# Kernel optimization log

Measured on AMD Instinct MI355X. Metric: run time of the kernel, lower is better.

Reference implementation:

```python
import jax, jax.numpy as jnp
import numpy as np

TEMPERATURE = 0.07
ALPHA = 1.0
SIGMOID_SCALE = 1.0
EPS = 1e-8

BSZ, N_VIEWS, D = 256, 2, 128


def setup_inputs() -> dict:
    key = jax.random.key(0)
    k1, k2, k3 = jax.random.split(key, 3)
    features = jax.random.normal(k1, (BSZ, N_VIEWS, D), dtype=jnp.float32)
    labels = jax.random.uniform(k2, (BSZ,), dtype=jnp.float32)  # continuous positions
    v_prog = jax.random.normal(k3, (D,), dtype=jnp.float32)     # learned direction param
    return {"features": features, "labels": labels, "v_prog": v_prog}


def _l2_normalize(x, axis, eps=1e-12):
    # matches F.normalize: x / clamp_min(||x||, eps)
    n = jnp.linalg.norm(x, axis=axis, keepdims=True)
    return x / jnp.maximum(n, eps)


def reference(features, labels, v_prog):
    bsz, n_views, d = features.shape
    # contrast_mode='all': torch.cat(torch.unbind(features, dim=1), dim=0)
    cf = jnp.concatenate([features[:, v] for v in range(n_views)], axis=0)  # (n, d)
    pos = jnp.tile(labels.reshape(-1, 1), (n_views, 1))                      # (n, 1)
    n = cf.shape[0]

    # ---------------- RAL loss ----------------
    f = _l2_normalize(cf, axis=1)
    sim = (f @ f.T) / TEMPERATURE                 # (n, n)
    pd = jnp.abs(pos - pos.T)                     # (n, n) |p_i - p_j|
    exp_sim = jnp.exp(sim)
    not_i = ~jnp.eye(n, dtype=bool)               # exclude k == i
    # mask3[i, j, k] = (pd[i,k] >= pd[i,j]) & (k != i)
    mask3 = (pd[:, None, :] >= pd[:, :, None]) & not_i[:, None, :]
    # denominator[i, j] = sum_k exp_sim[i, k] * mask3[i, j, k]  (fused masked reduction)
    denom = jnp.sum(jnp.where(mask3, exp_sim[:, None, :], 0.0), axis=2)
    loss_mat = -jnp.log(exp_sim / (denom + EPS))
    valid = not_i.astype(jnp.float32) * (denom > 0).astype(jnp.float32)
    soft_w = jax.nn.sigmoid(SIGMOID_SCALE * pd)   # apply_soft_weights=True
    cnt = valid.sum()
    ral = jnp.where(cnt > 0, (loss_mat * soft_w * valid).sum() / cnt, 0.0)

    # ---------------- OAL loss ----------------
    v = v_prog / (jnp.linalg.norm(v_prog) + EPS)
    mask = (pos < pos.T).astype(jnp.float32)      # mask[i,j] = p_i < p_j
    # cos[i,j] = (f_j - f_i) . v / ||f_j - f_i|| computed in O(n^2) without (n,n,d)
    proj = cf @ v                                  # (n,)
    sqn = jnp.sum(cf * cf, axis=1)                 # (n,)
    sqdist = jnp.maximum(sqn[:, None] + sqn[None, :] - 2.0 * (cf @ cf.T), 0.0)
    dist = jnp.sqrt(jnp.maximum(sqdist, 1e-24))    # clamp matches F.normalize eps behaviour
    cos = (proj[None, :] - proj[:, None]) / jnp.maximum(dist, 1e-12)
    cm = mask.sum()
    oal = jnp.where(cm > 0, -(cos * mask).sum() / cm, 0.0)

    return ral + ALPHA * oal
```

## Files before the change

kernel.cpp:

```cpp
#include <hip/hip_runtime.h>
#include <math.h>

#define NN 512
#define DD 128
#define TEMP_INV (1.0f / 0.07f)
#define EPSF 1e-8f

#define WS_VN   15
#define WS_SV   16
#define WS_RK   528
#define WS_PROJ 1040
#define WS_PART 1552
#define WS_G    4096

__global__ __launch_bounds__(256) void prep_kernel(
    const float* __restrict__ features,
    const float* __restrict__ labels,
    const float* __restrict__ v_prog,
    float* __restrict__ ws)
{
    const int b = blockIdx.x;
    const int t = threadIdx.x;
    if (b < 256) {
        __shared__ __align__(16) float a_s[32 * 132];
        __shared__ __align__(16) float b_s[32 * 132];
        const int tr = b >> 4, tc = b & 15;
        #pragma unroll
        for (int it = 0; it < 4; ++it) {
            const int fidx = t + 256 * it;
            const int rl = fidx >> 5, q = fidx & 31;
            const int ra = 32 * tr + rl, rb = 32 * tc + rl;
            float4 va = ((const float4*)features)[((ra & 255) * 2 + (ra >> 8)) * 32 + q];
            float4 vb = ((const float4*)features)[((rb & 255) * 2 + (rb >> 8)) * 32 + q];
            *(float4*)(a_s + rl * 132 + 4 * q) = va;
            *(float4*)(b_s + rl * 132 + 4 * q) = vb;
        }
        __syncthreads();
        const int my = (t >> 4) * 2, mx = (t & 15) * 2;
        float c00 = 0.f, c01 = 0.f, c10 = 0.f, c11 = 0.f;
        #pragma unroll 4
        for (int q = 0; q < 32; ++q) {
            float4 a0 = *(const float4*)(a_s + (my + 0) * 132 + 4 * q);
            float4 a1 = *(const float4*)(a_s + (my + 1) * 132 + 4 * q);
            float4 b0 = *(const float4*)(b_s + (mx + 0) * 132 + 4 * q);
            float4 b1 = *(const float4*)(b_s + (mx + 1) * 132 + 4 * q);
            c00 += a0.x*b0.x + a0.y*b0.y + a0.z*b0.z + a0.w*b0.w;
            c01 += a0.x*b1.x + a0.y*b1.y + a0.z*b1.z + a0.w*b1.w;
            c10 += a1.x*b0.x + a1.y*b0.y + a1.z*b0.z + a1.w*b0.w;
            c11 += a1.x*b1.x + a1.y*b1.y + a1.z*b1.z + a1.w*b1.w;
        }
        const int gr = 32 * tr + my, gc = 32 * tc + mx;
        ws[WS_G + (gr + 0) * NN + gc + 0] = c00;
        ws[WS_G + (gr + 0) * NN + gc + 1] = c01;
        ws[WS_G + (gr + 1) * NN + gc + 0] = c10;
        ws[WS_G + (gr + 1) * NN + gc + 1] = c11;
    } else if (b < 258) {
        __shared__ __align__(16) float vp_s[DD];
        if (t < DD) vp_s[t] = v_prog[t];
        __syncthreads();
        const int row = (b - 256) * 256 + t;
        const float4* src = (const float4*)features + ((row & 255) * 2 + (row >> 8)) * 32;
        const float4* v4 = (const float4*)vp_s;
        float p0 = 0.f, p1 = 0.f, p2 = 0.f, p3 = 0.f;
        #pragma unroll 8
        for (int q = 0; q < 32; ++q) {
            float4 a = src[q]; float4 v = v4[q];
            p0 += a.x*v.x; p1 += a.y*v.y; p2 += a.z*v.z; p3 += a.w*v.w;
        }
        ws[WS_PROJ + row] = (p0 + p1) + (p2 + p3);
    } else if (b == 258) {
        __shared__ float s0[4];
        float x = (t < DD) ? v_prog[t] : 0.f;
        float s = x * x;
        #pragma unroll
        for (int o = 32; o > 0; o >>= 1) s += __shfl_down(s, o);
        if ((t & 63) == 0) s0[t >> 6] = s;
        __syncthreads();
        if (t == 0) ws[WS_VN] = sqrtf(s0[0] + s0[1] + s0[2] + s0[3]) + EPSF;
    } else {
        __shared__ __align__(16) float pos_s[NN];
        const int k = (b - 259) * 256 + t;
        for (int m = t; m < NN; m += 256) pos_s[m] = labels[m & 255];
        __syncthreads();
        const float pk = pos_s[k];
        const float4* p4 = (const float4*)pos_s;
        int r = 0;
        #pragma unroll 8
        for (int q = 0; q < NN / 4; ++q) {
            float4 v = p4[q];
            const int m0 = 4 * q;
            r += (int)(v.x < pk) | ((int)(v.x == pk) & (int)(m0 + 0 < k));
            r += (int)(v.y < pk) | ((int)(v.y == pk) & (int)(m0 + 1 < k));
            r += (int)(v.z < pk) | ((int)(v.z == pk) & (int)(m0 + 2 < k));
            r += (int)(v.w < pk) | ((int)(v.w == pk) & (int)(m0 + 3 < k));
        }
        ws[WS_SV + r] = pk;
        ((int*)ws)[WS_RK + k] = r;
    }
}

__global__ __launch_bounds__(512) void main_kernel(
    const float* __restrict__ labels,
    float* __restrict__ ws)
{
    __shared__ float sv_s[NN];
    __shared__ float esS[NN];
    __shared__ float wtot[8];
    __shared__ float red_s[32];

    const int i = blockIdx.x;
    const int t = threadIdx.x;

    sv_s[t] = ws[WS_SV + t];
    const int rk_t = ((const int*)ws)[WS_RK + t];
    const int rk_i = ((const int*)ws)[WS_RK + i];
    const float g      = ws[WS_G + i * NN + t];
    const float sqn_i  = ws[WS_G + i * NN + i];
    const float sqn_k  = ws[WS_G + t * NN + t];
    const float proj_i = ws[WS_PROJ + i];
    const float proj_k = ws[WS_PROJ + t];
    const float vn     = ws[WS_VN];
    const float pos_i  = labels[i & 255];
    const float pos_k  = labels[t & 255];

    const float inv_ni = 1.0f / fmaxf(sqrtf(sqn_i), 1e-12f);
    const float inv_nk = 1.0f / fmaxf(sqrtf(sqn_k), 1e-12f);
    const float sim    = g * inv_ni * inv_nk * TEMP_INV;
    const float es     = (t == i) ? 0.0f : __expf(sim);
    esS[rk_t] = es;

    float oal_sum = 0.f, oal_cnt = 0.f;
    if (pos_i < pos_k) {
        float sqd  = fmaxf(sqn_i + sqn_k - 2.0f * g, 0.0f);
        float dist = sqrtf(fmaxf(sqd, 1e-24f));
        oal_sum = (proj_k - proj_i) / (vn * fmaxf(dist, 1e-12f));
        oal_cnt = 1.0f;
    }
    __syncthreads();

    float s = esS[t];
    #pragma unroll
    for (int off = 1; off < 64; off <<= 1) {
        float u = __shfl_up(s, off);
        if ((t & 63) >= off) s += u;
    }
    const int wid = t >> 6;
    if ((t & 63) == 63) wtot[wid] = s;
    __syncthreads();
    float woff = 0.f;
    for (int w = 0; w < wid; ++w) woff += wtot[w];
    esS[t] = s + woff;
    __syncthreads();
    const float total = esS[NN - 1];

    const float thr = fabsf(pos_i - pos_k);
    int lo = 0, hi = rk_i;
    #pragma unroll
    for (int step = 256; step > 0; step >>= 1) {
        if (lo + step <= rk_i && !(fabsf(pos_i - sv_s[lo + step - 1]) < thr)) lo += step;
        if (hi + step <= NN   &&  (fabsf(pos_i - sv_s[hi + step - 1]) < thr)) hi += step;
    }

    const float pe_lo = (lo > 0) ? esS[lo - 1] : 0.0f;
    const float pe_hi = (hi > 0) ? esS[hi - 1] : 0.0f;
    float ral_sum = 0.f, ral_cnt = 0.f;
    if (t != i) {
        float denom = fmaxf(pe_lo + (total - pe_hi), es);
        const float sw = 1.0f / (1.0f + __expf(-thr));
        ral_sum = (__logf(denom + EPSF) - sim) * sw;
        ral_cnt = 1.0f;
    }

    #pragma unroll
    for (int o = 32; o > 0; o >>= 1) {
        ral_sum += __shfl_down(ral_sum, o);
        ral_cnt += __shfl_down(ral_cnt, o);
        oal_sum += __shfl_down(oal_sum, o);
        oal_cnt += __shfl_down(oal_cnt, o);
    }
    if ((t & 63) == 0) {
        red_s[wid*4+0] = ral_sum; red_s[wid*4+1] = ral_cnt;
        red_s[wid*4+2] = oal_sum; red_s[wid*4+3] = oal_cnt;
    }
    __syncthreads();
    if (t == 0) {
        float rs = 0.f, rc = 0.f, os = 0.f, oc = 0.f;
        #pragma unroll
        for (int w = 0; w < 8; ++w) {
            rs += red_s[w*4+0]; rc += red_s[w*4+1];
            os += red_s[w*4+2]; oc += red_s[w*4+3];
        }
        float* pp = ws + WS_PART + i * 4;
        pp[0] = rs; pp[1] = rc; pp[2] = os; pp[3] = oc;
    }
}

__global__ __launch_bounds__(256) void final_kernel(
    const float* __restrict__ ws, float* __restrict__ out)
{
    __shared__ double dred[16];
    const int t = threadIdx.x;
    double rs = 0.0, rc = 0.0, os = 0.0, oc = 0.0;
    for (int b = t; b < NN; b += 256) {
        const float* p = ws + WS_PART + b * 4;
        rs += (double)p[0]; rc += (double)p[1];
        os += (double)p[2]; oc += (double)p[3];
    }
    #pragma unroll
    for (int o = 32; o > 0; o >>= 1) {
        rs += __shfl_down(rs, o);
        rc += __shfl_down(rc, o);
        os += __shfl_down(os, o);
        oc += __shfl_down(oc, o);
    }
    if ((t & 63) == 0) {
        int w = t >> 6;
        dred[w*4+0] = rs; dred[w*4+1] = rc;
        dred[w*4+2] = os; dred[w*4+3] = oc;
    }
    __syncthreads();
    if (t == 0) {
        double RS = 0, RC = 0, OS = 0, OC = 0;
        for (int w = 0; w < 4; ++w) {
            RS += dred[w*4+0]; RC += dred[w*4+1];
            OS += dred[w*4+2]; OC += dred[w*4+3];
        }
        double ral = (RC > 0.0) ? RS / RC : 0.0;
        double oal = (OC > 0.0) ? -(OS / OC) : 0.0;
        out[0] = (float)(ral + oal);
    }
}

extern "C" void kernel_launch(void* const* d_in, const int* in_sizes, int n_in,
                              void* d_out, int out_size, void* d_ws, size_t ws_size,
                              hipStream_t stream) {
    const float* features = (const float*)d_in[0];
    const float* labels   = (const float*)d_in[1];
    const float* v_prog   = (const float*)d_in[2];
    float* ws  = (float*)d_ws;
    float* out = (float*)d_out;

    hipLaunchKernelGGL(prep_kernel,  dim3(261), dim3(256), 0, stream,
                       features, labels, v_prog, ws);
    hipLaunchKernelGGL(main_kernel,  dim3(NN),  dim3(512), 0, stream, labels, ws);
    hipLaunchKernelGGL(final_kernel, dim3(1),   dim3(256), 0, stream, ws, out);
}
```

Baseline: 32.59 us.

## Use 16x16 Gram tiles with 1024 blocks and store squared norms contiguously

The Gram-matrix part of the prep kernel now uses 16x16 output tiles, one element per thread, across 1024 blocks instead of 32x32 tiles with 2x2 per thread across 256 blocks. This spreads the work over more CUs (MI355X has 256), at the cost of more redundant feature loads per output and less register reuse. Diagonal entries are also written to a contiguous squared-norm array. The main kernel reads the norms from that array instead of doing strided diagonal loads from the Gram matrix.

```diff
diff --git a/kernel.cpp b/kernel.cpp
--- a/kernel.cpp
+++ b/kernel.cpp
@@ -10,7 +10,8 @@
 #define WS_SV   16
 #define WS_RK   528
 #define WS_PROJ 1040
-#define WS_PART 1552
+#define WS_SQN  1552
+#define WS_PART 2064
 #define WS_G    4096
 
 __global__ __launch_bounds__(256) void prep_kernel(
@@ -21,44 +22,42 @@
 {
     const int b = blockIdx.x;
     const int t = threadIdx.x;
-    if (b < 256) {
-        __shared__ __align__(16) float a_s[32 * 132];
-        __shared__ __align__(16) float b_s[32 * 132];
-        const int tr = b >> 4, tc = b & 15;
-        #pragma unroll
-        for (int it = 0; it < 4; ++it) {
-            const int fidx = t + 256 * it;
-            const int rl = fidx >> 5, q = fidx & 31;
-            const int ra = 32 * tr + rl, rb = 32 * tc + rl;
-            float4 va = ((const float4*)features)[((ra & 255) * 2 + (ra >> 8)) * 32 + q];
-            float4 vb = ((const float4*)features)[((rb & 255) * 2 + (rb >> 8)) * 32 + q];
-            *(float4*)(a_s + rl * 132 + 4 * q) = va;
-            *(float4*)(b_s + rl * 132 + 4 * q) = vb;
-        }
-        __syncthreads();
-        const int my = (t >> 4) * 2, mx = (t & 15) * 2;
-        float c00 = 0.f, c01 = 0.f, c10 = 0.f, c11 = 0.f;
-        #pragma unroll 4
+    if (b < 1024) {
+        __shared__ __align__(16) float a_s[16 * 132];
+        __shared__ __align__(16) float b_s[16 * 132];
+        const int tr = b >> 5, tc = b & 31;
+        {
+            const int rl = t >> 5, q = t & 31;
+            const int ra0 = 16 * tr + rl, rb0 = 16 * tc + rl;
+            const int ra1 = ra0 + 8,      rb1 = rb0 + 8;
+            float4 va0 = ((const float4*)features)[((ra0 & 255) * 2 + (ra0 >> 8)) * 32 + q];
+            float4 vb0 = ((const float4*)features)[((rb0 & 255) * 2 + (rb0 >> 8)) * 32 + q];
+            float4 va1 = ((const float4*)features)[((ra1 & 255) * 2 + (ra1 >> 8)) * 32 + q];
+            float4 vb1 = ((const float4*)features)[((rb1 & 255) * 2 + (rb1 >> 8)) * 32 + q];
+            *(float4*)(a_s + (rl + 0) * 132 + 4 * q) = va0;
+            *(float4*)(b_s + (rl + 0) * 132 + 4 * q) = vb0;
+            *(float4*)(a_s + (rl + 8) * 132 + 4 * q) = va1;
+            *(float4*)(b_s + (rl + 8) * 132 + 4 * q) = vb1;
+        }
+        __syncthreads();
+        const int y = t >> 4, x = t & 15;
+        const float4* arow = (const float4*)(a_s + y * 132);
+        const float4* brow = (const float4*)(b_s + x * 132);
+        float c0 = 0.f, c1 = 0.f, c2 = 0.f, c3 = 0.f;
+        #pragma unroll 8
         for (int q = 0; q < 32; ++q) {
-            float4 a0 = *(const float4*)(a_s + (my + 0) * 132 + 4 * q);
-            float4 a1 = *(const float4*)(a_s + (my + 1) * 132 + 4 * q);
-            float4 b0 = *(const float4*)(b_s + (mx + 0) * 132 + 4 * q);
-            float4 b1 = *(const float4*)(b_s + (mx + 1) * 132 + 4 * q);
-            c00 += a0.x*b0.x + a0.y*b0.y + a0.z*b0.z + a0.w*b0.w;
-            c01 += a0.x*b1.x + a0.y*b1.y + a0.z*b1.z + a0.w*b1.w;
-            c10 += a1.x*b0.x + a1.y*b0.y + a1.z*b0.z + a1.w*b0.w;
-            c11 += a1.x*b1.x + a1.y*b1.y + a1.z*b1.z + a1.w*b1.w;
-        }
-        const int gr = 32 * tr + my, gc = 32 * tc + mx;
-        ws[WS_G + (gr + 0) * NN + gc + 0] = c00;
-        ws[WS_G + (gr + 0) * NN + gc + 1] = c01;
-        ws[WS_G + (gr + 1) * NN + gc + 0] = c10;
-        ws[WS_G + (gr + 1) * NN + gc + 1] = c11;
-    } else if (b < 258) {
+            float4 a = arow[q]; float4 v = brow[q];
+            c0 += a.x * v.x; c1 += a.y * v.y; c2 += a.z * v.z; c3 += a.w * v.w;
+        }
+        const float c = (c0 + c1) + (c2 + c3);
+        const int gr = 16 * tr + y, gc = 16 * tc + x;
+        ws[WS_G + gr * NN + gc] = c;
+        if (gr == gc) ws[WS_SQN + gr] = c;
+    } else if (b < 1026) {
         __shared__ __align__(16) float vp_s[DD];
         if (t < DD) vp_s[t] = v_prog[t];
         __syncthreads();
-        const int row = (b - 256) * 256 + t;
+        const int row = (b - 1024) * 256 + t;
         const float4* src = (const float4*)features + ((row & 255) * 2 + (row >> 8)) * 32;
         const float4* v4 = (const float4*)vp_s;
         float p0 = 0.f, p1 = 0.f, p2 = 0.f, p3 = 0.f;
@@ -68,7 +67,7 @@
             p0 += a.x*v.x; p1 += a.y*v.y; p2 += a.z*v.z; p3 += a.w*v.w;
         }
         ws[WS_PROJ + row] = (p0 + p1) + (p2 + p3);
-    } else if (b == 258) {
+    } else if (b == 1026) {
         __shared__ float s0[4];
         float x = (t < DD) ? v_prog[t] : 0.f;
         float s = x * x;
@@ -79,7 +78,7 @@
         if (t == 0) ws[WS_VN] = sqrtf(s0[0] + s0[1] + s0[2] + s0[3]) + EPSF;
     } else {
         __shared__ __align__(16) float pos_s[NN];
-        const int k = (b - 259) * 256 + t;
+        const int k = (b - 1027) * 256 + t;
         for (int m = t; m < NN; m += 256) pos_s[m] = labels[m & 255];
         __syncthreads();
         const float pk = pos_s[k];
@@ -115,8 +114,8 @@
     const int rk_t = ((const int*)ws)[WS_RK + t];
     const int rk_i = ((const int*)ws)[WS_RK + i];
     const float g      = ws[WS_G + i * NN + t];
-    const float sqn_i  = ws[WS_G + i * NN + i];
-    const float sqn_k  = ws[WS_G + t * NN + t];
+    const float sqn_i  = ws[WS_SQN + i];
+    const float sqn_k  = ws[WS_SQN + t];
     const float proj_i = ws[WS_PROJ + i];
     const float proj_k = ws[WS_PROJ + t];
     const float vn     = ws[WS_VN];
@@ -240,8 +239,8 @@
     float* ws  = (float*)d_ws;
     float* out = (float*)d_out;
 
-    hipLaunchKernelGGL(prep_kernel,  dim3(261), dim3(256), 0, stream,
+    hipLaunchKernelGGL(prep_kernel,  dim3(1029), dim3(256), 0, stream,
                        features, labels, v_prog, ws);
-    hipLaunchKernelGGL(main_kernel,  dim3(NN),  dim3(512), 0, stream, labels, ws);
-    hipLaunchKernelGGL(final_kernel, dim3(1),   dim3(256), 0, stream, ws, out);
-}
+    hipLaunchKernelGGL(main_kernel,  dim3(NN),   dim3(512), 0, stream, labels, ws);
+    hipLaunchKernelGGL(final_kernel, dim3(1),    dim3(256), 0, stream, ws, out);
+}
```

Result: faster. 30.98 us (-4.9%).
